# Performance work log

Hardware: AMD Instinct MI355X
Metric: run time of the kernel (lower is better)

Reference implementation:

```python
import jax, jax.numpy as jnp
import numpy as np


def setup_inputs() -> dict:
    key = jax.random.key(0)
    ks = jax.random.split(key, 8)
    B, D, H, W = 4, 96, 64, 64
    K, N, R = 4, 16, 6
    return {
        "x": jax.random.normal(ks[0], (B, D, H, W), jnp.float32),
        "x_proj_weight": jax.random.normal(ks[1], (K, R + 2 * N, D), jnp.float32) * 0.05,
        "dt_projs_weight": jax.random.normal(ks[2], (K, D, R), jnp.float32) * 0.1,
        "dt_projs_bias": jax.random.normal(ks[3], (K, D), jnp.float32) * 0.1,
        "A_logs": jax.random.uniform(ks[4], (K * D, N), jnp.float32),
        "Ds": jax.random.normal(ks[5], (K * D,), jnp.float32),
        "ln_weight": jnp.ones((D,), jnp.float32),
        "ln_bias": jnp.zeros((D,), jnp.float32),
    }


def reference(x, x_proj_weight, dt_projs_weight, dt_projs_bias, A_logs, Ds, ln_weight, ln_bias):
    B, D, H, W = x.shape
    K, _, R = dt_projs_weight.shape
    N = A_logs.shape[1]
    L = H * W

    # ---- CrossScan: 4 traversal orders (row-major, col-major, and their reverses) ----
    xf = x.reshape(B, D, L)                                   # row-major
    xt = jnp.transpose(x, (0, 1, 3, 2)).reshape(B, D, L)      # col-major
    xs = jnp.stack([xf, xt, xf[..., ::-1], xt[..., ::-1]], axis=1)  # (B, K, D, L)

    # ---- input-dependent projections ----
    x_dbl = jnp.einsum('bkdl,kcd->bkcl', xs, x_proj_weight)   # (B, K, R+2N, L)
    dts, Bs, Cs = jnp.split(x_dbl, [R, R + N], axis=2)        # Bs/Cs: (B, K, N, L)
    dts = jnp.einsum('bkrl,kdr->bkdl', dts, dt_projs_weight)  # (B, K, D, L)

    A = -jnp.exp(A_logs).reshape(K, D, N)                     # (K, D, N)
    delta = jax.nn.softplus(dts + dt_projs_bias[None, :, :, None])  # (B, K, D, L)

    # ---- selective (S6) scan over L ----
    def step(h, inp):
        d_t, u_t, B_t, C_t = inp  # (B,K,D) (B,K,D) (B,K,N) (B,K,N)
        dA = jnp.exp(d_t[..., None] * A[None])                # (B,K,D,N)
        h = h * dA + (d_t * u_t)[..., None] * B_t[:, :, None, :]
        y_t = jnp.einsum('bkdn,bkn->bkd', h, C_t)
        return h, y_t

    h0 = jnp.zeros((B, K, D, N), x.dtype)
    seq = (jnp.moveaxis(delta, -1, 0), jnp.moveaxis(xs, -1, 0),
           jnp.moveaxis(Bs, -1, 0), jnp.moveaxis(Cs, -1, 0))
    _, ys = jax.lax.scan(step, h0, seq)                       # (L, B, K, D)
    ys = jnp.moveaxis(ys, 0, -1)                              # (B, K, D, L)
    ys = ys + Ds.reshape(K, D)[None, :, :, None] * xs         # skip term D*u

    # ---- CrossMerge: undo the 4 traversal orders and sum ----
    m = ys[:, 0:2] + ys[:, 2:4][..., ::-1]                    # (B, 2, D, L)
    y = m[:, 0] + jnp.transpose(m[:, 1].reshape(B, D, W, H), (0, 1, 3, 2)).reshape(B, D, L)

    # ---- out_norm (LayerNorm over channels, v0 path) ----
    y = jnp.transpose(y, (0, 2, 1))                           # (B, L, D)
    mu = y.mean(-1, keepdims=True)
    var = y.var(-1, keepdims=True)
    y = (y - mu) / jnp.sqrt(var + 1e-5) * ln_weight + ln_bias
    return y.reshape(B, H, W, D)
```

## Files before the change

### kernel.cpp

```cpp
#include <hip/hip_runtime.h>
#include <hip/hip_fp16.h>
#include <math.h>

#define B_ 4
#define D_ 96
#define H_ 64
#define W_ 64
#define L_ 4096
#define K_ 4
#define N_ 16
#define R_ 6
#define C_ 38
#define SSX 128
#define CLSX (L_ / SSX)
#define CH_ (B_ * K_ * D_ * N_)

#if defined(__has_builtin)
#if __has_builtin(__builtin_amdgcn_exp2f)
#define EXP2F(x) __builtin_amdgcn_exp2f(x)
#else
#define EXP2F(x) exp2f(x)
#endif
#else
#define EXP2F(x) exp2f(x)
#endif
#define LOG2E 1.44269504f

#define SW(d) ((((d) >> 2) & 7) << 2)

__device__ __forceinline__ int src_idx(int k, int l) {
    int m = (k >= 2) ? (L_ - 1 - l) : l;
    if (k & 1) return ((m & 63) << 6) | (m >> 6);
    return m;
}

__device__ __forceinline__ float softplus_f(float a) {
    return (a > 15.f) ? a : __logf(1.f + __expf(a));
}

__device__ __forceinline__ ushort f2h(float v) {
    return __half_as_ushort(__float2half_rn(v));
}

__device__ __forceinline__ void load_h8(const __half* p, float* out) {
    uint4 raw = *(const uint4*)p;
    const __half2* h2 = (const __half2*)&raw;
#pragma unroll
    for (int i = 0; i < 4; ++i) {
        float2 f = __half22float2(h2[i]);
        out[2 * i] = f.x;
        out[2 * i + 1] = f.y;
    }
}

__device__ __forceinline__ float4 load_h4(const __half* p) {
    uint2 raw = *(const uint2*)p;
    const __half2* h2 = (const __half2*)&raw;
    float2 a = __half22float2(h2[0]);
    float2 b = __half22float2(h2[1]);
    return make_float4(a.x, a.y, b.x, b.y);
}

__global__ __launch_bounds__(256) void transpose_kernel(
    const float* __restrict__ x,
    __half* __restrict__ xs2)
{
    int bid = blockIdx.x;
    int b = bid / (3 * 64);
    int rest = bid % (3 * 64);
    int dblk = rest / 64, lblk = rest % 64;
    int d0 = dblk * 32;
    int l0 = lblk * 64;
    int tid = threadIdx.x;

    __shared__ float s_t[32][65];

    for (int i = tid; i < 32 * 64; i += 256) {
        int d = i >> 6, l = i & 63;
        s_t[d][l] = x[((long)b * D_ + d0 + d) * L_ + l0 + l];
    }
    __syncthreads();

    for (int i = tid; i < 64 * 32; i += 256) {
        int l = i >> 5, d = i & 31;
        __half v = __float2half_rn(s_t[d][l]);
        xs2[((long)b * L_ + l0 + l) * D_ + d0 + d] = v;
        xs2[((long)(B_ + b) * L_ + l * 64 + lblk) * D_ + d0 + d] = v;
    }
}

__global__ __launch_bounds__(256) void proj_scan_kernel(
    const __half* __restrict__ xs2,
    const float* __restrict__ xpw,
    const float* __restrict__ wdt,
    const float* __restrict__ bdt,
    const float* __restrict__ A_logs,
    __half* __restrict__ delta,
    __half* __restrict__ Bsb,
    __half* __restrict__ Csb,
    float* __restrict__ pAarr,
    float* __restrict__ hharr)
{
    const int TL = 64;
    const int tiles = L_ / TL;
    int bid = blockIdx.x;
    int bk = bid / tiles;
    int tile = bid % tiles;
    int b = bk / K_, k = bk % K_;
    int l0 = tile * TL;
    int tid = threadIdx.x;

    __shared__ __align__(16) float  s_wpT[D_ * 40];
    __shared__ __align__(16) __half s_xs[D_ * 68];
    __shared__ __align__(16) float  s_wdt[R_ * D_];
    __shared__ __align__(16) float  s_bias[D_];
    __shared__ __align__(16) float  s_dts[R_ * 68];
    __shared__ __align__(16) float  s_B[TL * N_];

    for (int i = tid; i < C_ * D_; i += 256) {
        int d = i / C_, c = i % C_;
        int cp = (c < 6) ? c : c + 2;
        s_wpT[d * 40 + cp] = xpw[(k * C_ + c) * D_ + d];
    }
    for (int i = tid; i < 96; i += 256) {
        s_wpT[i * 40 + 6] = 0.f;
        s_wpT[i * 40 + 7] = 0.f;
    }
    for (int i = tid; i < R_ * D_; i += 256) {
        int r = i / D_, d = i % D_;
        s_wdt[i] = wdt[(k * D_ + d) * R_ + r];
    }
    if (tid < D_) s_bias[tid] = bdt[k * D_ + tid];

    const __half* xsp = xs2 + (long)((k & 1) * B_ + b) * L_ * D_;
    for (int i = tid; i < TL * 24; i += 256) {
        int lt = i / 24, dq = i % 24;
        int row = (k < 2) ? (l0 + lt) : (L_ - 1 - l0 - lt);
        uint2 raw = *(const uint2*)(xsp + (long)row * D_ + dq * 4);
        const __half* hv = (const __half*)&raw;
        int d0 = dq * 4;
        s_xs[(d0 + 0) * 68 + (lt ^ SW(d0 + 0))] = hv[0];
        s_xs[(d0 + 1) * 68 + (lt ^ SW(d0 + 1))] = hv[1];
        s_xs[(d0 + 2) * 68 + (lt ^ SW(d0 + 2))] = hv[2];
        s_xs[(d0 + 3) * 68 + (lt ^ SW(d0 + 3))] = hv[3];
    }
    __syncthreads();

    long base = (long)bk * L_ + l0;

    int ct = tid >> 4;
    int lt4 = (tid & 15) * 4;
    if (ct < 10) {
        int cp0 = ct * 4;
        float acc[4][4];
#pragma unroll
        for (int i = 0; i < 4; ++i)
#pragma unroll
            for (int j = 0; j < 4; ++j) acc[i][j] = 0.f;
#pragma unroll 4
        for (int d = 0; d < D_; ++d) {
            float4 wv = *(const float4*)(&s_wpT[d * 40 + cp0]);
            float4 xv = load_h4(&s_xs[d * 68 + (lt4 ^ SW(d))]);
            float wa[4] = {wv.x, wv.y, wv.z, wv.w};
            float xa[4] = {xv.x, xv.y, xv.z, xv.w};
#pragma unroll
            for (int ci = 0; ci < 4; ++ci)
#pragma unroll
                for (int li = 0; li < 4; ++li)
                    acc[ci][li] += wa[ci] * xa[li];
        }
        if (ct == 0) {
#pragma unroll
            for (int ci = 0; ci < 4; ++ci)
                *(float4*)(&s_dts[ci * 68 + lt4]) =
                    make_float4(acc[ci][0], acc[ci][1], acc[ci][2], acc[ci][3]);
        } else if (ct == 1) {
#pragma unroll
            for (int ci = 0; ci < 2; ++ci)
                *(float4*)(&s_dts[(4 + ci) * 68 + lt4]) =
                    make_float4(acc[ci][0], acc[ci][1], acc[ci][2], acc[ci][3]);
        } else if (ct < 6) {
            int n0 = cp0 - 8;
#pragma unroll
            for (int li = 0; li < 4; ++li) {
                ushort4 hv;
                hv.x = f2h(acc[0][li]); hv.y = f2h(acc[1][li]);
                hv.z = f2h(acc[2][li]); hv.w = f2h(acc[3][li]);
                *(ushort4*)(&Bsb[(base + lt4 + li) * N_ + n0]) = hv;
                *(float4*)(&s_B[(lt4 + li) * N_ + n0]) =
                    make_float4(acc[0][li], acc[1][li], acc[2][li], acc[3][li]);
            }
        } else {
            int n0 = cp0 - 24;
#pragma unroll
            for (int li = 0; li < 4; ++li) {
                ushort4 hv;
                hv.x = f2h(acc[0][li]); hv.y = f2h(acc[1][li]);
                hv.z = f2h(acc[2][li]); hv.w = f2h(acc[3][li]);
                *(ushort4*)(&Csb[(base + lt4 + li) * N_ + n0]) = hv;
            }
        }
    }
    __syncthreads();

    for (int tt = tid; tt < 24 * 16; tt += 256) {
        int dt = tt % 24, lt4b = (tt / 24) * 4;
        int d0 = dt * 4;
        float4 bias = *(const float4*)(&s_bias[d0]);
        float acc[4][4];
#pragma unroll
        for (int li = 0; li < 4; ++li) {
            acc[li][0] = bias.x; acc[li][1] = bias.y;
            acc[li][2] = bias.z; acc[li][3] = bias.w;
        }
#pragma unroll
        for (int r = 0; r < R_; ++r) {
            float4 wv = *(const float4*)(&s_wdt[r * D_ + d0]);
            float4 tv = *(const float4*)(&s_dts[r * 68 + lt4b]);
            float wa[4] = {wv.x, wv.y, wv.z, wv.w};
            float ta[4] = {tv.x, tv.y, tv.z, tv.w};
#pragma unroll
            for (int li = 0; li < 4; ++li)
#pragma unroll
                for (int di = 0; di < 4; ++di)
                    acc[li][di] += ta[li] * wa[di];
        }
#pragma unroll
        for (int li = 0; li < 4; ++li) {
            ushort4 o;
            o.x = f2h(softplus_f(acc[li][0]));
            o.y = f2h(softplus_f(acc[li][1]));
            o.z = f2h(softplus_f(acc[li][2]));
            o.w = f2h(softplus_f(acc[li][3]));
            *(ushort4*)(&delta[(base + lt4b + li) * D_ + d0]) = o;
        }
    }

    if (tid < 192) {
        int sub = tid / 96;
        int dd = tid % 96;
        int j = tile * 2 + sub;
        int kd = k * D_ + dd;

        float A2[16];
        {
            const float4* ap = (const float4*)(A_logs + kd * N_);
#pragma unroll
            for (int q = 0; q < 4; ++q) {
                float4 a = ap[q];
                A2[q * 4 + 0] = -__expf(a.x) * LOG2E;
                A2[q * 4 + 1] = -__expf(a.y) * LOG2E;
                A2[q * 4 + 2] = -__expf(a.z) * LOG2E;
                A2[q * 4 + 3] = -__expf(a.w) * LOG2E;
            }
        }
        float wdtr[R_];
#pragma unroll
        for (int r = 0; r < R_; ++r) wdtr[r] = s_wdt[r * D_ + dd];
        float biasv = s_bias[dd];
        int sw = SW(dd);

        float h[16];
#pragma unroll
        for (int i = 0; i < 16; ++i) h[i] = 0.f;
        float sdel = 0.f;

#pragma unroll 4
        for (int t = 0; t < CLSX; ++t) {
            int lt = sub * CLSX + t;
            float acc = biasv;
#pragma unroll
            for (int r = 0; r < R_; ++r) acc += wdtr[r] * s_dts[r * 68 + lt];
            float del = softplus_f(acc);
            float u = __half2float(s_xs[dd * 68 + (lt ^ sw)]);
            float Bv[16];
            *(float4*)(Bv + 0)  = *(const float4*)(&s_B[lt * N_ + 0]);
            *(float4*)(Bv + 4)  = *(const float4*)(&s_B[lt * N_ + 4]);
            *(float4*)(Bv + 8)  = *(const float4*)(&s_B[lt * N_ + 8]);
            *(float4*)(Bv + 12) = *(const float4*)(&s_B[lt * N_ + 12]);
            sdel += del;
            float delu = del * u;
#pragma unroll
            for (int i = 0; i < 16; ++i) {
                float dA = EXP2F(del * A2[i]);
                h[i] = h[i] * dA + delu * Bv[i];
            }
        }

        long sbase = (long)j * CH_ + (long)(bk * D_ + dd) * N_;
#pragma unroll
        for (int q = 0; q < 4; ++q) {
            *(float4*)(pAarr + sbase + q * 4) =
                make_float4(EXP2F(A2[q * 4 + 0] * sdel), EXP2F(A2[q * 4 + 1] * sdel),
                            EXP2F(A2[q * 4 + 2] * sdel), EXP2F(A2[q * 4 + 3] * sdel));
            *(float4*)(hharr + sbase + q * 4) =
                make_float4(h[q * 4], h[q * 4 + 1], h[q * 4 + 2], h[q * 4 + 3]);
        }
    }
}

__global__ __launch_bounds__(256) void scan_combine(
    const float* __restrict__ pAarr,
    float* __restrict__ hharr)
{
    int c = blockIdx.x * 256 + threadIdx.x;
    float h = 0.f;
#pragma unroll 16
    for (int j = 0; j < SSX; ++j) {
        long idx = (long)j * CH_ + c;
        float tmp = hharr[idx];
        float pa  = pAarr[idx];
        hharr[idx] = h;
        h = tmp + pa * h;
    }
}

__global__ __launch_bounds__(384) void scan_part2_pair(
    const float* __restrict__ A_logs,
    const float* __restrict__ Ds,
    const __half* __restrict__ xs2,
    const __half* __restrict__ delta,
    const __half* __restrict__ Bsb,
    const __half* __restrict__ Csb,
    const float* __restrict__ hharr,
    float* __restrict__ ypair)
{
    __shared__ float s_y[2][CLSX][D_];

    int bid = blockIdx.x;
    int b = bid / (2 * SSX);
    int rest = bid % (2 * SSX);
    int p = rest / SSX;
    int j = rest % SSX;
    int tid = threadIdx.x;
    int g = tid / 192;
    int r = tid % 192;
    int dd = r >> 1;
    int half = r & 1;
    int n0 = half * 8;

    int kdir = p + 2 * g;
    int bk = b * K_ + kdir;
    int jj = g ? (SSX - 1 - j) : j;
    int l0s = jj * CLSX;
    int kd = kdir * D_ + dd;

    float A2[8];
    {
        const float4* ap = (const float4*)(A_logs + kd * N_ + n0);
        float4 a0 = ap[0], a1 = ap[1];
        A2[0] = -__expf(a0.x) * LOG2E; A2[1] = -__expf(a0.y) * LOG2E;
        A2[2] = -__expf(a0.z) * LOG2E; A2[3] = -__expf(a0.w) * LOG2E;
        A2[4] = -__expf(a1.x) * LOG2E; A2[5] = -__expf(a1.y) * LOG2E;
        A2[6] = -__expf(a1.z) * LOG2E; A2[7] = -__expf(a1.w) * LOG2E;
    }
    float Dv = Ds[kd];

    const __half* dp = delta + ((long)bk * L_ + l0s) * D_ + dd;
    const __half* bp = Bsb + ((long)bk * L_ + l0s) * N_ + n0;
    const __half* cp = Csb + ((long)bk * L_ + l0s) * N_ + n0;
    const __half* xsp = xs2 + (long)(p * B_ + b) * L_ * D_;
    long urow0 = g ? ((long)j * CLSX + CLSX - 1) : (long)l0s;
    long ustep = g ? -D_ : D_;
    const __half* up = xsp + urow0 * D_ + dd;

    float h[8];
    {
        long sbase = (long)jj * CH_ + (long)(bk * D_ + dd) * N_ + n0;
        float4 h0 = *(const float4*)(hharr + sbase);
        float4 h1 = *(const float4*)(hharr + sbase + 4);
        h[0] = h0.x; h[1] = h0.y; h[2] = h0.z; h[3] = h0.w;
        h[4] = h1.x; h[5] = h1.y; h[6] = h1.z; h[7] = h1.w;
    }

#pragma unroll 4
    for (int t = 0; t < CLSX; ++t) {
        float del = __half2float(dp[(long)t * D_]);
        float u   = __half2float(up[(long)t * ustep]);
        float Bv[8], Cv[8];
        load_h8(bp + t * N_, Bv);
        load_h8(cp + t * N_, Cv);
        float delu = del * u;
        float yv = 0.f;
#pragma unroll
        for (int i = 0; i < 8; ++i) {
            float dA = EXP2F(del * A2[i]);
            h[i] = h[i] * dA + delu * Bv[i];
            yv += h[i] * Cv[i];
        }
        yv += __shfl_xor(yv, 1);
        if (half == 0) {
            int tpos = g ? (CLSX - 1 - t) : t;
            s_y[g][tpos][dd] = yv + Dv * u;
        }
    }
    __syncthreads();

    float* yo = ypair + ((long)(p * B_ + b) * L_ + (long)j * CLSX) * D_;
    for (int i = tid; i < CLSX * 24; i += 384) {
        int lt = i / 24, dq = i % 24;
        int d0 = dq * 4;
        float4 o = make_float4(s_y[0][lt][d0 + 0] + s_y[1][lt][d0 + 0],
                               s_y[0][lt][d0 + 1] + s_y[1][lt][d0 + 1],
                               s_y[0][lt][d0 + 2] + s_y[1][lt][d0 + 2],
                               s_y[0][lt][d0 + 3] + s_y[1][lt][d0 + 3]);
        *(float4*)(yo + (long)lt * D_ + d0) = o;
    }
}

__global__ __launch_bounds__(256) void ln_merge_kernel(
    const float* __restrict__ ypair,
    const float* __restrict__ lnw,
    const float* __restrict__ lnb,
    float* __restrict__ out)
{
    int wid = (blockIdx.x * 256 + threadIdx.x) >> 6;
    int lane = threadIdx.x & 63;
    int b = wid / L_;
    int m = wid % L_;
    int mt = ((m & 63) << 6) | (m >> 6);

    const float* y0 = ypair + ((long)b * L_ + m) * D_;
    const float* y1 = ypair + ((long)(B_ + b) * L_ + mt) * D_;

    float v0 = y0[lane] + y1[lane];
    float v1 = (lane < 32) ? (y0[64 + lane] + y1[64 + lane]) : 0.f;

    float s  = v0 + v1;
    float s2 = v0 * v0 + v1 * v1;
#pragma unroll
    for (int mm = 1; mm < 64; mm <<= 1) {
        s  += __shfl_xor(s, mm);
        s2 += __shfl_xor(s2, mm);
    }
    float mu  = s * (1.f / D_);
    float var = s2 * (1.f / D_) - mu * mu;
    float rstd = rsqrtf(var + 1e-5f);

    long obase = (long)wid * D_;
    out[obase + lane] = (v0 - mu) * rstd * lnw[lane] + lnb[lane];
    if (lane < 32)
        out[obase + 64 + lane] = (v1 - mu) * rstd * lnw[64 + lane] + lnb[64 + lane];
}

__global__ __launch_bounds__(256) void proj_legacy(
    const float* __restrict__ x,
    const float* __restrict__ xpw,
    const float* __restrict__ wdt,
    const float* __restrict__ bdt,
    float* __restrict__ delta,
    float* __restrict__ Bsb,
    float* __restrict__ Csb)
{
    const int TL = 64;
    const int tiles = L_ / TL;
    int bid = blockIdx.x;
    int bk = bid / tiles;
    int tile = bid % tiles;
    int b = bk / K_, k = bk % K_;
    int l0 = tile * TL;
    int tid = threadIdx.x;

    __shared__ float s_wp[C_ * D_];
    __shared__ float s_wdt[R_ * D_];
    __shared__ float s_bias[D_];
    __shared__ float s_xs[D_ * (TL + 1)];
    __shared__ float s_xdbl[C_ * (TL + 1)];

    for (int i = tid; i < C_ * D_; i += 256) s_wp[i] = xpw[k * C_ * D_ + i];
    for (int i = tid; i < R_ * D_; i += 256) {
        int r = i / D_, d = i % D_;
        s_wdt[i] = wdt[(k * D_ + d) * R_ + r];
    }
    if (tid < D_) s_bias[tid] = bdt[k * D_ + tid];
    for (int i = tid; i < D_ * TL; i += 256) {
        int d = i / TL, lt = i % TL;
        s_xs[d * (TL + 1) + lt] = x[(b * D_ + d) * L_ + src_idx(k, l0 + lt)];
    }
    __syncthreads();

    for (int idx = tid; idx < C_ * TL; idx += 256) {
        int c = idx / TL, lt = idx % TL;
        const float* wr = &s_wp[c * D_];
        float acc = 0.f;
#pragma unroll 8
        for (int d = 0; d < D_; ++d) acc += wr[d] * s_xs[d * (TL + 1) + lt];
        s_xdbl[c * (TL + 1) + lt] = acc;
    }
    __syncthreads();

    long base = (long)bk * L_ + l0;
    for (int idx = tid; idx < TL * D_; idx += 256) {
        int lt = idx / D_, d = idx % D_;
        float acc = s_bias[d];
#pragma unroll
        for (int r = 0; r < R_; ++r)
            acc += s_wdt[r * D_ + d] * s_xdbl[r * (TL + 1) + lt];
        delta[(base + lt) * D_ + d] = softplus_f(acc);
    }
    for (int idx = tid; idx < TL * 2 * N_; idx += 256) {
        int lt = idx / (2 * N_), c2 = idx % (2 * N_);
        float v = s_xdbl[(R_ + c2) * (TL + 1) + lt];
        if (c2 < N_) Bsb[(base + lt) * N_ + c2] = v;
        else         Csb[(base + lt) * N_ + (c2 - N_)] = v;
    }
}

__global__ __launch_bounds__(64) void scan_serial(
    const float* __restrict__ x,
    const float* __restrict__ A_logs,
    const float* __restrict__ Ds,
    const float* __restrict__ delta,
    const float* __restrict__ Bsb,
    const float* __restrict__ Csb,
    float* __restrict__ ys)
{
    const int chans = D_ / 4;
    int bid = blockIdx.x;
    int bk = bid / chans;
    int d0 = (bid % chans) * 4;
    int b = bk / K_, k = bk % K_;
    int lane = threadIdx.x;
    int g = lane >> 4, n = lane & 15;
    int d = d0 + g;
    int kd = k * D_ + d;

    float A  = -__expf(A_logs[kd * N_ + n]);
    float Dv = Ds[kd];
    const float* dptr = delta + ((long)bk * L_) * D_ + d;
    const float* bptr = Bsb + (long)bk * L_ * N_ + n;
    const float* cptr = Csb + (long)bk * L_ * N_ + n;
    const float* xptr = x + ((long)b * D_ + d) * L_;
    float* yptr = ys + ((long)bk * L_) * D_ + d;

    float h = 0.f;
#pragma unroll 4
    for (int l = 0; l < L_; ++l) {
        float del = dptr[(long)l * D_];
        float u   = xptr[src_idx(k, l)];
        float Bt  = bptr[l * N_];
        float Ct  = cptr[l * N_];
        float dA  = __expf(del * A);
        h = h * dA + del * u * Bt;
        float yv = h * Ct;
        yv += __shfl_xor(yv, 1);
        yv += __shfl_xor(yv, 2);
        yv += __shfl_xor(yv, 4);
        yv += __shfl_xor(yv, 8);
        if (n == 0) yptr[(long)l * D_] = yv + Dv * u;
    }
}

__global__ __launch_bounds__(256) void merge_ln_kernel(
    const float* __restrict__ ys,
    const float* __restrict__ lnw,
    const float* __restrict__ lnb,
    float* __restrict__ out)
{
    int wid = (blockIdx.x * 256 + threadIdx.x) >> 6;
    int lane = threadIdx.x & 63;
    int b = wid / L_;
    int l = wid % L_;
    int lt = ((l & 63) << 6) | (l >> 6);

    long base0 = ((long)(b * K_ + 0) * L_ + l) * D_;
    long base2 = ((long)(b * K_ + 2) * L_ + (L_ - 1 - l)) * D_;
    long base1 = ((long)(b * K_ + 1) * L_ + lt) * D_;
    long base3 = ((long)(b * K_ + 3) * L_ + (L_ - 1 - lt)) * D_;

    int dA = lane;
    int dB = lane + 64;
    float v0 = ys[base0 + dA] + ys[base2 + dA] + ys[base1 + dA] + ys[base3 + dA];
    float v1 = 0.f;
    if (dB < D_)
        v1 = ys[base0 + dB] + ys[base2 + dB] + ys[base1 + dB] + ys[base3 + dB];

    float s  = v0 + v1;
    float s2 = v0 * v0 + v1 * v1;
#pragma unroll
    for (int m = 1; m < 64; m <<= 1) {
        s  += __shfl_xor(s, m);
        s2 += __shfl_xor(s2, m);
    }
    float mu  = s * (1.f / D_);
    float var = s2 * (1.f / D_) - mu * mu;
    float rstd = rsqrtf(var + 1e-5f);

    long obase = ((long)b * L_ + l) * D_;
    out[obase + dA] = (v0 - mu) * rstd * lnw[dA] + lnb[dA];
    if (dB < D_)
        out[obase + dB] = (v1 - mu) * rstd * lnw[dB] + lnb[dB];
}

extern "C" void kernel_launch(void* const* d_in, const int* in_sizes, int n_in,
                              void* d_out, int out_size, void* d_ws, size_t ws_size,
                              hipStream_t stream) {
    const float* x      = (const float*)d_in[0];
    const float* xpw    = (const float*)d_in[1];
    const float* wdt    = (const float*)d_in[2];
    const float* bdt    = (const float*)d_in[3];
    const float* A_logs = (const float*)d_in[4];
    const float* Ds     = (const float*)d_in[5];
    const float* lnw    = (const float*)d_in[6];
    const float* lnb    = (const float*)d_in[7];
    float* out = (float*)d_out;

    const long n_delta = (long)B_ * K_ * L_ * D_;
    const long n_bc    = (long)B_ * K_ * L_ * N_;
    const long n_bld   = (long)B_ * L_ * D_;
    const long n_sum   = (long)SSX * CH_;

    char* wsb = (char*)d_ws;
    __half* delta = (__half*)wsb;
    __half* Bsb   = (__half*)(wsb + n_delta * 2);
    __half* Csb   = (__half*)(wsb + n_delta * 2 + n_bc * 2);
    __half* xs2   = (__half*)(wsb + n_delta * 2 + n_bc * 4);
    float*  ypair = (float*)(wsb + n_delta * 2 + n_bc * 4 + 2 * n_bld * 2);
    float*  hharr = ypair + 2 * n_bld;
    float*  pAarr = ypair;
    size_t need = (size_t)(n_delta * 2 + n_bc * 4 + 2 * n_bld * 2) +
                  (size_t)(2 * n_bld + n_sum) * 4;

    if (ws_size >= need) {
        transpose_kernel<<<B_ * 3 * 64, 256, 0, stream>>>(x, xs2);
        proj_scan_kernel<<<B_ * K_ * (L_ / 64), 256, 0, stream>>>(
            xs2, xpw, wdt, bdt, A_logs, delta, Bsb, Csb, pAarr, hharr);
        scan_combine<<<CH_ / 256, 256, 0, stream>>>(pAarr, hharr);
        scan_part2_pair<<<B_ * 2 * SSX, 384, 0, stream>>>(
            A_logs, Ds, xs2, delta, Bsb, Csb, hharr, ypair);
        ln_merge_kernel<<<(B_ * L_) / 4, 256, 0, stream>>>(ypair, lnw, lnb, out);
    } else {
        float* ws = (float*)d_ws;
        float* deltaf = ws;
        float* Bsb2   = deltaf + n_delta;
        float* Csb2   = Bsb2 + n_bc;
        float* ys2    = Csb2 + n_bc;
        proj_legacy<<<B_ * K_ * (L_ / 64), 256, 0, stream>>>(
            x, xpw, wdt, bdt, deltaf, Bsb2, Csb2);
        scan_serial<<<B_ * K_ * (D_ / 4), 64, 0, stream>>>(
            x, A_logs, Ds, deltaf, Bsb2, Csb2, ys2);
        merge_ln_kernel<<<(B_ * L_) / 4, 256, 0, stream>>>(ys2, lnw, lnb, out);
    }
}
```

Before: 172.5 us.

## Widen proj_scan to 384 threads, split state halves, store chunk summaries in fp16

The projection/scan kernel now launches 384 threads. The projection GEMM uses 2-channel tiles across more threads, the dt loop gives one tile per thread, and the chunk-local scan splits the 16 state elements into two halves per thread so all 384 threads work. Chunk decay products and partial states are now written as fp16 instead of fp32, which halves traffic in scan_combine and scan_part2. This raises parallelism and lowers register pressure per thread, but fp16 storage of carried states and decay factors adds precision risk.

```diff
diff --git a/kernel.cpp b/kernel.cpp
--- a/kernel.cpp
+++ b/kernel.cpp
@@ -53,6 +53,15 @@
     }
 }
 
+__device__ __forceinline__ void store_h8(__half* p, const float* v) {
+    uint4 raw;
+    __half2* h2 = (__half2*)&raw;
+#pragma unroll
+    for (int i = 0; i < 4; ++i)
+        h2[i] = __floats2half2_rn(v[2 * i], v[2 * i + 1]);
+    *(uint4*)p = raw;
+}
+
 __device__ __forceinline__ float4 load_h4(const __half* p) {
     uint2 raw = *(const uint2*)p;
     const __half2* h2 = (const __half2*)&raw;
@@ -89,7 +98,7 @@
     }
 }
 
-__global__ __launch_bounds__(256) void proj_scan_kernel(
+__global__ __launch_bounds__(384) void proj_scan_kernel(
     const __half* __restrict__ xs2,
     const float* __restrict__ xpw,
     const float* __restrict__ wdt,
@@ -98,8 +107,8 @@
     __half* __restrict__ delta,
     __half* __restrict__ Bsb,
     __half* __restrict__ Csb,
-    float* __restrict__ pAarr,
-    float* __restrict__ hharr)
+    __half* __restrict__ pAarr,
+    __half* __restrict__ hharr)
 {
     const int TL = 64;
     const int tiles = L_ / TL;
@@ -117,23 +126,23 @@
     __shared__ __align__(16) float  s_dts[R_ * 68];
     __shared__ __align__(16) float  s_B[TL * N_];
 
-    for (int i = tid; i < C_ * D_; i += 256) {
+    for (int i = tid; i < C_ * D_; i += 384) {
         int d = i / C_, c = i % C_;
         int cp = (c < 6) ? c : c + 2;
         s_wpT[d * 40 + cp] = xpw[(k * C_ + c) * D_ + d];
     }
-    for (int i = tid; i < 96; i += 256) {
+    for (int i = tid; i < 96; i += 384) {
         s_wpT[i * 40 + 6] = 0.f;
         s_wpT[i * 40 + 7] = 0.f;
     }
-    for (int i = tid; i < R_ * D_; i += 256) {
+    for (int i = tid; i < R_ * D_; i += 384) {
         int r = i / D_, d = i % D_;
         s_wdt[i] = wdt[(k * D_ + d) * R_ + r];
     }
     if (tid < D_) s_bias[tid] = bdt[k * D_ + tid];
 
     const __half* xsp = xs2 + (long)((k & 1) * B_ + b) * L_ * D_;
-    for (int i = tid; i < TL * 24; i += 256) {
+    for (int i = tid; i < TL * 24; i += 384) {
         int lt = i / 24, dq = i % 24;
         int row = (k < 2) ? (l0 + lt) : (L_ - 1 - l0 - lt);
         uint2 raw = *(const uint2*)(xsp + (long)row * D_ + dq * 4);
@@ -150,61 +159,54 @@
 
     int ct = tid >> 4;
     int lt4 = (tid & 15) * 4;
-    if (ct < 10) {
-        int cp0 = ct * 4;
-        float acc[4][4];
-#pragma unroll
-        for (int i = 0; i < 4; ++i)
+    if (ct < 20 && ct != 3) {
+        int cp0 = ct * 2;
+        float acc[2][4];
+#pragma unroll
+        for (int i = 0; i < 2; ++i)
 #pragma unroll
             for (int j = 0; j < 4; ++j) acc[i][j] = 0.f;
 #pragma unroll 4
         for (int d = 0; d < D_; ++d) {
-            float4 wv = *(const float4*)(&s_wpT[d * 40 + cp0]);
+            float2 wv = *(const float2*)(&s_wpT[d * 40 + cp0]);
             float4 xv = load_h4(&s_xs[d * 68 + (lt4 ^ SW(d))]);
-            float wa[4] = {wv.x, wv.y, wv.z, wv.w};
+            float wa[2] = {wv.x, wv.y};
             float xa[4] = {xv.x, xv.y, xv.z, xv.w};
 #pragma unroll
-            for (int ci = 0; ci < 4; ++ci)
+            for (int ci = 0; ci < 2; ++ci)
 #pragma unroll
                 for (int li = 0; li < 4; ++li)
                     acc[ci][li] += wa[ci] * xa[li];
         }
-        if (ct == 0) {
-#pragma unroll
-            for (int ci = 0; ci < 4; ++ci)
-                *(float4*)(&s_dts[ci * 68 + lt4]) =
+        if (ct < 3) {
+#pragma unroll
+            for (int ci = 0; ci < 2; ++ci)
+                *(float4*)(&s_dts[(cp0 + ci) * 68 + lt4]) =
                     make_float4(acc[ci][0], acc[ci][1], acc[ci][2], acc[ci][3]);
-        } else if (ct == 1) {
-#pragma unroll
-            for (int ci = 0; ci < 2; ++ci)
-                *(float4*)(&s_dts[(4 + ci) * 68 + lt4]) =
-                    make_float4(acc[ci][0], acc[ci][1], acc[ci][2], acc[ci][3]);
-        } else if (ct < 6) {
+        } else if (ct < 12) {
             int n0 = cp0 - 8;
 #pragma unroll
             for (int li = 0; li < 4; ++li) {
-                ushort4 hv;
+                ushort2 hv;
                 hv.x = f2h(acc[0][li]); hv.y = f2h(acc[1][li]);
-                hv.z = f2h(acc[2][li]); hv.w = f2h(acc[3][li]);
-                *(ushort4*)(&Bsb[(base + lt4 + li) * N_ + n0]) = hv;
-                *(float4*)(&s_B[(lt4 + li) * N_ + n0]) =
-                    make_float4(acc[0][li], acc[1][li], acc[2][li], acc[3][li]);
+                *(ushort2*)(&Bsb[(base + lt4 + li) * N_ + n0]) = hv;
+                *(float2*)(&s_B[(lt4 + li) * N_ + n0]) =
+                    make_float2(acc[0][li], acc[1][li]);
             }
         } else {
             int n0 = cp0 - 24;
 #pragma unroll
             for (int li = 0; li < 4; ++li) {
-                ushort4 hv;
+                ushort2 hv;
                 hv.x = f2h(acc[0][li]); hv.y = f2h(acc[1][li]);
-                hv.z = f2h(acc[2][li]); hv.w = f2h(acc[3][li]);
-                *(ushort4*)(&Csb[(base + lt4 + li) * N_ + n0]) = hv;
+                *(ushort2*)(&Csb[(base + lt4 + li) * N_ + n0]) = hv;
             }
         }
     }
     __syncthreads();
 
-    for (int tt = tid; tt < 24 * 16; tt += 256) {
-        int dt = tt % 24, lt4b = (tt / 24) * 4;
+    {
+        int dt = tid % 24, lt4b = (tid / 24) * 4;
         int d0 = dt * 4;
         float4 bias = *(const float4*)(&s_bias[d0]);
         float acc[4][4];
@@ -236,33 +238,33 @@
         }
     }
 
-    if (tid < 192) {
-        int sub = tid / 96;
-        int dd = tid % 96;
+    {
+        int sub = tid / 192;
+        int r = tid % 192;
+        int dd = r >> 1;
+        int half = r & 1;
+        int n0h = half * 8;
         int j = tile * 2 + sub;
         int kd = k * D_ + dd;
 
-        float A2[16];
+        float A2[8];
         {
-            const float4* ap = (const float4*)(A_logs + kd * N_);
-#pragma unroll
-            for (int q = 0; q < 4; ++q) {
-                float4 a = ap[q];
-                A2[q * 4 + 0] = -__expf(a.x) * LOG2E;
-                A2[q * 4 + 1] = -__expf(a.y) * LOG2E;
-                A2[q * 4 + 2] = -__expf(a.z) * LOG2E;
-                A2[q * 4 + 3] = -__expf(a.w) * LOG2E;
-            }
+            const float4* ap = (const float4*)(A_logs + kd * N_ + n0h);
+            float4 a0 = ap[0], a1 = ap[1];
+            A2[0] = -__expf(a0.x) * LOG2E; A2[1] = -__expf(a0.y) * LOG2E;
+            A2[2] = -__expf(a0.z) * LOG2E; A2[3] = -__expf(a0.w) * LOG2E;
+            A2[4] = -__expf(a1.x) * LOG2E; A2[5] = -__expf(a1.y) * LOG2E;
+            A2[6] = -__expf(a1.z) * LOG2E; A2[7] = -__expf(a1.w) * LOG2E;
         }
         float wdtr[R_];
 #pragma unroll
-        for (int r = 0; r < R_; ++r) wdtr[r] = s_wdt[r * D_ + dd];
+        for (int rr = 0; rr < R_; ++rr) wdtr[rr] = s_wdt[rr * D_ + dd];
         float biasv = s_bias[dd];
         int sw = SW(dd);
 
-        float h[16];
-#pragma unroll
-        for (int i = 0; i < 16; ++i) h[i] = 0.f;
+        float h[8];
+#pragma unroll
+        for (int i = 0; i < 8; ++i) h[i] = 0.f;
         float sdel = 0.f;
 
 #pragma unroll 4
@@ -270,47 +272,42 @@
             int lt = sub * CLSX + t;
             float acc = biasv;
 #pragma unroll
-            for (int r = 0; r < R_; ++r) acc += wdtr[r] * s_dts[r * 68 + lt];
+            for (int rr = 0; rr < R_; ++rr) acc += wdtr[rr] * s_dts[rr * 68 + lt];
             float del = softplus_f(acc);
             float u = __half2float(s_xs[dd * 68 + (lt ^ sw)]);
-            float Bv[16];
-            *(float4*)(Bv + 0)  = *(const float4*)(&s_B[lt * N_ + 0]);
-            *(float4*)(Bv + 4)  = *(const float4*)(&s_B[lt * N_ + 4]);
-            *(float4*)(Bv + 8)  = *(const float4*)(&s_B[lt * N_ + 8]);
-            *(float4*)(Bv + 12) = *(const float4*)(&s_B[lt * N_ + 12]);
+            float Bv[8];
+            *(float4*)(Bv + 0) = *(const float4*)(&s_B[lt * N_ + n0h]);
+            *(float4*)(Bv + 4) = *(const float4*)(&s_B[lt * N_ + n0h + 4]);
             sdel += del;
             float delu = del * u;
 #pragma unroll
-            for (int i = 0; i < 16; ++i) {
+            for (int i = 0; i < 8; ++i) {
                 float dA = EXP2F(del * A2[i]);
                 h[i] = h[i] * dA + delu * Bv[i];
             }
         }
 
-        long sbase = (long)j * CH_ + (long)(bk * D_ + dd) * N_;
-#pragma unroll
-        for (int q = 0; q < 4; ++q) {
-            *(float4*)(pAarr + sbase + q * 4) =
-                make_float4(EXP2F(A2[q * 4 + 0] * sdel), EXP2F(A2[q * 4 + 1] * sdel),
-                            EXP2F(A2[q * 4 + 2] * sdel), EXP2F(A2[q * 4 + 3] * sdel));
-            *(float4*)(hharr + sbase + q * 4) =
-                make_float4(h[q * 4], h[q * 4 + 1], h[q * 4 + 2], h[q * 4 + 3]);
-        }
+        long sbase = (long)j * CH_ + (long)(bk * D_ + dd) * N_ + n0h;
+        float pv[8];
+#pragma unroll
+        for (int i = 0; i < 8; ++i) pv[i] = EXP2F(A2[i] * sdel);
+        store_h8(pAarr + sbase, pv);
+        store_h8(hharr + sbase, h);
     }
 }
 
 __global__ __launch_bounds__(256) void scan_combine(
-    const float* __restrict__ pAarr,
-    float* __restrict__ hharr)
+    const __half* __restrict__ pAarr,
+    __half* __restrict__ hharr)
 {
     int c = blockIdx.x * 256 + threadIdx.x;
     float h = 0.f;
 #pragma unroll 16
     for (int j = 0; j < SSX; ++j) {
         long idx = (long)j * CH_ + c;
-        float tmp = hharr[idx];
-        float pa  = pAarr[idx];
-        hharr[idx] = h;
+        float tmp = __half2float(hharr[idx]);
+        float pa  = __half2float(pAarr[idx]);
+        hharr[idx] = __float2half_rn(h);
         h = tmp + pa * h;
     }
 }
@@ -322,7 +319,7 @@
     const __half* __restrict__ delta,
     const __half* __restrict__ Bsb,
     const __half* __restrict__ Csb,
-    const float* __restrict__ hharr,
+    const __half* __restrict__ hharr,
     float* __restrict__ ypair)
 {
     __shared__ float s_y[2][CLSX][D_];
@@ -365,13 +362,7 @@
     const __half* up = xsp + urow0 * D_ + dd;
 
     float h[8];
-    {
-        long sbase = (long)jj * CH_ + (long)(bk * D_ + dd) * N_ + n0;
-        float4 h0 = *(const float4*)(hharr + sbase);
-        float4 h1 = *(const float4*)(hharr + sbase + 4);
-        h[0] = h0.x; h[1] = h0.y; h[2] = h0.z; h[3] = h0.w;
-        h[4] = h1.x; h[5] = h1.y; h[6] = h1.z; h[7] = h1.w;
-    }
+    load_h8(hharr + (long)jj * CH_ + (long)(bk * D_ + dd) * N_ + n0, h);
 
 #pragma unroll 4
     for (int t = 0; t < CLSX; ++t) {
@@ -616,14 +607,14 @@
     __half* Csb   = (__half*)(wsb + n_delta * 2 + n_bc * 2);
     __half* xs2   = (__half*)(wsb + n_delta * 2 + n_bc * 4);
     float*  ypair = (float*)(wsb + n_delta * 2 + n_bc * 4 + 2 * n_bld * 2);
-    float*  hharr = ypair + 2 * n_bld;
-    float*  pAarr = ypair;
+    __half* hharr = (__half*)((char*)ypair + 2 * n_bld * 4);
+    __half* pAarr = (__half*)ypair;
     size_t need = (size_t)(n_delta * 2 + n_bc * 4 + 2 * n_bld * 2) +
-                  (size_t)(2 * n_bld + n_sum) * 4;
+                  (size_t)(2 * n_bld) * 4 + (size_t)n_sum * 2;
 
     if (ws_size >= need) {
         transpose_kernel<<<B_ * 3 * 64, 256, 0, stream>>>(x, xs2);
-        proj_scan_kernel<<<B_ * K_ * (L_ / 64), 256, 0, stream>>>(
+        proj_scan_kernel<<<B_ * K_ * (L_ / 64), 384, 0, stream>>>(
             xs2, xpw, wdt, bdt, A_logs, delta, Bsb, Csb, pAarr, hharr);
         scan_combine<<<CH_ / 256, 256, 0, stream>>>(pAarr, hharr);
         scan_part2_pair<<<B_ * 2 * SSX, 384, 0, stream>>>(
```

Result: slower. 181.6 us (+5.3%).
